# Kernel tuning notes

Measured on AMD Instinct MI355X. Metric: run time of the kernel, lower is better.

## Reference

```python
import jax, jax.numpy as jnp
import numpy as np


def _conv1x1(x, w, b=None):
    # x: [B,C,H,W], w: [O,C]
    y = jnp.einsum('bchw,oc->bohw', x, w)
    if b is not None:
        y = y + b[None, :, None, None]
    return y


def _conv3x3_dilated(x, w, b, dil):
    p = dil  # padding == dilation keeps spatial size for 3x3 kernels
    y = jax.lax.conv_general_dilated(
        x, w, window_strides=(1, 1), padding=((p, p), (p, p)),
        rhs_dilation=(dil, dil), dimension_numbers=('NCHW', 'OIHW', 'NCHW'))
    return y + b[None, :, None, None]


def _upsample2x_align_corners(x):
    # bilinear, align_corners=True, scale factor 2
    B, C, H, W = x.shape
    oh, ow = 2 * H, 2 * W
    ys = jnp.linspace(0.0, H - 1.0, oh)
    xs = jnp.linspace(0.0, W - 1.0, ow)
    y0 = jnp.floor(ys).astype(jnp.int32)
    x0 = jnp.floor(xs).astype(jnp.int32)
    y1 = jnp.minimum(y0 + 1, H - 1)
    x1 = jnp.minimum(x0 + 1, W - 1)
    wy = (ys - y0)[None, None, :, None]
    wx = (xs - x0)[None, None, None, :]
    gt = x[:, :, y0, :]
    gb = x[:, :, y1, :]
    top = gt[:, :, :, x0] * (1 - wx) + gt[:, :, :, x1] * wx
    bot = gb[:, :, :, x0] * (1 - wx) + gb[:, :, :, x1] * wx
    return top * (1 - wy) + bot * wy


def _gr(ftr, ck_w, ck_b, avg_w, max_w, gcn_w):
    # GR module: attention-diagonal graph conv with degree normalization
    B, C, H, W = ftr.shape
    HW = H * W
    # ChannelAttention_diag -> diagonal entries cw: [B, M]
    avg = ftr.mean(axis=(2, 3))
    mx = ftr.max(axis=(2, 3))
    cw = jax.nn.sigmoid(jax.nn.relu(avg @ avg_w.T) + jax.nn.relu(mx @ max_w.T))  # [B,M]
    k = jax.nn.relu(_conv1x1(ftr, ck_w, ck_b)).reshape(B, -1, HW)  # [B,M,HW]
    q = jnp.swapaxes(k, 1, 2)  # [B,HW,M]
    # A = sigmoid(q @ diag(cw) @ k); degree d = rowsum(A)^(-1/2)
    A = jax.nn.sigmoid(jnp.einsum('bim,bm,bmj->bij', q, cw, k))  # [B,HW,HW]
    d = A.sum(axis=2) ** -0.5  # [B,HW]
    P = d[:, :, None] * q  # D^{-1/2} @ q, [B,HW,M]
    X = jnp.swapaxes(ftr.reshape(B, C, HW), 1, 2)  # [B,HW,C]
    PtX = jnp.einsum('bjm,bjc->bmc', P, X)  # [B,M,C]
    LX = X - jnp.einsum('bim,bmc->bic', P, cw[:, :, None] * PtX)
    Y = X + LX @ gcn_w  # GCN (no bias)
    return jnp.swapaxes(Y, 1, 2).reshape(B, C, H, W)


def setup_inputs() -> dict:
    key = jax.random.key(0)
    ks = jax.random.split(key, 20)
    B, C = 64, 1024
    Cq = C // 4  # 256
    Mi = Cq // 2  # 128, ChannelAttention inter channels
    s = 0.02
    inp = {
        'x_cur': jax.random.normal(ks[0], (B, C, 16, 16), jnp.float32),
        'x_lat': jax.random.normal(ks[1], (B, C, 8, 8), jnp.float32),
        'conv_w': jax.random.normal(ks[2], (Cq, C), jnp.float32) * s,
        'conv_b': jax.random.normal(ks[3], (Cq,), jnp.float32) * s,
        'conv1_w': jax.random.normal(ks[4], (C, Cq), jnp.float32) * s,
        'conv1_b': jax.random.normal(ks[5], (C,), jnp.float32) * s,
        'conv3_w': jax.random.normal(ks[6], (C, 3 * Cq), jnp.float32) * s,
        'conv3_b': jax.random.normal(ks[7], (C,), jnp.float32) * s,
        'rate0_w': jax.random.normal(ks[8], (Cq, C, 3, 3), jnp.float32) * s,
        'rate0_b': jax.random.normal(ks[9], (Cq,), jnp.float32) * s,
        'rate1_w': jax.random.normal(ks[10], (Cq, C, 3, 3), jnp.float32) * s,
        'rate1_b': jax.random.normal(ks[11], (Cq,), jnp.float32) * s,
        'rate2_w': jax.random.normal(ks[12], (Cq, C, 3, 3), jnp.float32) * s,
        'rate2_b': jax.random.normal(ks[13], (Cq,), jnp.float32) * s,
        'gr_ck_w': jax.random.normal(ks[14], (Mi, Cq), jnp.float32) * s,
        'gr_ck_b': jax.random.normal(ks[15], (Mi,), jnp.float32) * s,
        'gr_avg_w': jax.random.normal(ks[16], (Mi, Cq), jnp.float32) * s,
        'gr_max_w': jax.random.normal(ks[17], (Mi, Cq), jnp.float32) * s,
        'gr_gcn_w': jax.random.normal(ks[18], (Cq, Cq), jnp.float32) * s,
        'pre': 1,
    }
    return inp


def reference(x_cur, x_lat, conv_w, conv_b, conv1_w, conv1_b, conv3_w, conv3_b,
              rate0_w, rate0_b, rate1_w, rate1_b, rate2_w, rate2_b,
              gr_ck_w, gr_ck_b, gr_avg_w, gr_max_w, gr_gcn_w, pre):
    # pre == 1 path of Graph_aspp.forward
    gr_args = (gr_ck_w, gr_ck_b, gr_avg_w, gr_max_w, gr_gcn_w)
    x_sum = x_cur * _upsample2x_align_corners(x_lat) + x_cur
    f1 = _conv3x3_dilated(x_sum, rate0_w, rate0_b, 1) + _conv1x1(x_sum, conv_w, conv_b)
    x1 = _gr(f1, *gr_args)
    feature = _conv1x1(f1, conv1_w, conv1_b) + x_sum
    f2 = _conv3x3_dilated(feature, rate1_w, rate1_b, 2) + _conv1x1(feature, conv_w, conv_b)
    x2 = _gr(f2, *gr_args)
    feature = _conv1x1(f2, conv1_w, conv1_b) + x_sum
    f3 = _conv3x3_dilated(feature, rate2_w, rate2_b, 4) + _conv1x1(feature, conv_w, conv_b)
    x3 = _gr(f3, *gr_args)
    cat = jnp.concatenate((x1, x2, x3), axis=1)
    return _conv1x1(cat, conv3_w, conv3_b)
```

## Files before the change

### kernel.cpp

```cpp
#include <hip/hip_runtime.h>

typedef unsigned short ushort_t;
typedef unsigned int uint32;
typedef __attribute__((ext_vector_type(8))) unsigned short ushort8;
typedef __attribute__((ext_vector_type(8))) __bf16 bf16x8;
typedef __attribute__((ext_vector_type(4))) float f32x4;

__device__ __forceinline__ ushort_t f2b(float f) {
    union { float f; uint32 u; } v; v.f = f;
    uint32 r = v.u + 0x7fffu + ((v.u >> 16) & 1u);
    return (ushort_t)(r >> 16);
}
__device__ __forceinline__ float b2f(ushort_t b) {
    union { uint32 u; float f; } v; v.u = ((uint32)b) << 16;
    return v.f;
}
__device__ __forceinline__ float sigm(float x) { return 1.f / (1.f + __expf(-x)); }

__device__ __forceinline__ void gload_lds16(const void* g, void* l) {
    __builtin_amdgcn_global_load_lds(
        (__attribute__((address_space(1))) void*)g,
        (__attribute__((address_space(3))) void*)l, 16, 0, 0);
}

constexpr int EPI_RELU  = 1;
constexpr int EPI_FQ    = 2;
constexpr int EPI_SIG   = 3;
constexpr int EPI_XG    = 4;
constexpr int EPI_NEGCW = 5;
constexpr int EPI_Y     = 6;
constexpr int EPI_OUTT  = 7;

struct GemmP {
    const ushort_t* A; const ushort_t* B;
    const ushort_t* A2; const ushort_t* B2;
    long long aBatch, bBatch, a2Batch, b2Batch;
    int lda, ldb, lda2, ldb2;
    int Ksub, kSplit, dil;
    const float* bias;
    const ushort_t* res; long long resBatch; int ldres;
    ushort_t* obf; long long oBatch; int ldo;
    ushort_t* obf2;
    float* of32;
    const float* cw;
    const float* rscale;
    float* dsum;
    const ushort_t* zpage;
};

__global__ __launch_bounds__(256) void gemm_big(GemmP p) {
    __shared__ __align__(16) ushort_t aT[128 * 64];
    __shared__ __align__(16) ushort_t bT[128 * 64];
    const int tid = threadIdx.x;
    const int z = blockIdx.z;
    const int m0 = blockIdx.x * 128, n0 = blockIdx.y * 128;
    const int lane = tid & 63, wid = tid >> 6;
    const int l15 = lane & 15, l16 = lane >> 4;
    const int wr = wid >> 1, wc = wid & 1;
    const int lrow = lane >> 3;
    const int sgran = (lane & 7) ^ lrow;

    int ayy[4], axx[4];
    const ushort_t* aBase[4];
    const ushort_t* bBase[4];
#pragma unroll
    for (int i = 0; i < 4; ++i) {
        int row = wid * 32 + i * 8 + lrow;
        int m = m0 + row;
        int bb = m >> 8;
        ayy[i] = (m >> 4) & 15; axx[i] = m & 15;
        aBase[i] = p.A + (long long)bb * 262144 + sgran * 8;
        bBase[i] = p.B + (long long)(n0 + row) * p.ldb + sgran * 8;
    }

    f32x4 acc[4][4];
#pragma unroll
    for (int i = 0; i < 4; ++i)
#pragma unroll
        for (int j = 0; j < 4; ++j) acc[i][j] = (f32x4){0.f, 0.f, 0.f, 0.f};

    const int gk0 = z * p.kSplit;
    const int ntap = p.Ksub >> 10;
    for (int ti = 0; ti < ntap; ++ti) {
        const int tap = (gk0 >> 10) + ti;
        int dy = 0, dx = 0;
        if (tap < 9) { int ky = tap / 3; dy = (ky - 1) * p.dil; dx = (tap - ky * 3 - 1) * p.dil; }
        const ushort_t* gaA[4];
        const ushort_t* gaB[4];
#pragma unroll
        for (int i = 0; i < 4; ++i) {
            int iy = ayy[i] + dy, ix = axx[i] + dx;
            bool ok = ((unsigned)iy < 16u) && ((unsigned)ix < 16u);
            gaA[i] = ok ? (aBase[i] + (((iy << 4) + ix) << 10)) : (p.zpage + sgran * 8);
            gaB[i] = bBase[i] + (tap << 10);
        }
        for (int kk = 0; kk < 16; ++kk) {
            const int kin = kk << 6;
#pragma unroll
            for (int i = 0; i < 4; ++i)
                gload_lds16(gaA[i] + kin, &aT[(wid * 32 + i * 8) * 64]);
#pragma unroll
            for (int i = 0; i < 4; ++i)
                gload_lds16(gaB[i] + kin, &bT[(wid * 32 + i * 8) * 64]);
            asm volatile("s_waitcnt vmcnt(0)" ::: "memory");
            __syncthreads();
#pragma unroll
            for (int ks = 0; ks < 2; ++ks) {
                bf16x8 af[4], bfr[4];
#pragma unroll
                for (int mi = 0; mi < 4; ++mi) {
                    int rr = wr * 64 + mi * 16 + l15;
                    int cc = (ks * 32 + l16 * 8) ^ ((rr & 7) << 3);
                    af[mi] = __builtin_bit_cast(bf16x8, *(const ushort8*)&aT[rr * 64 + cc]);
                }
#pragma unroll
                for (int ni = 0; ni < 4; ++ni) {
                    int rr = wc * 64 + ni * 16 + l15;
                    int cc = (ks * 32 + l16 * 8) ^ ((rr & 7) << 3);
                    bfr[ni] = __builtin_bit_cast(bf16x8, *(const ushort8*)&bT[rr * 64 + cc]);
                }
#pragma unroll
                for (int mi = 0; mi < 4; ++mi)
#pragma unroll
                    for (int ni = 0; ni < 4; ++ni)
                        acc[mi][ni] = __builtin_amdgcn_mfma_f32_16x16x32_bf16(af[mi], bfr[ni], acc[mi][ni], 0, 0, 0);
            }
            __syncthreads();
        }
    }
#pragma unroll
    for (int mi = 0; mi < 4; ++mi)
#pragma unroll
        for (int ni = 0; ni < 4; ++ni) {
            int gcol = n0 + wc * 64 + ni * 16 + l15;
            int growb = m0 + wr * 64 + mi * 16 + l16 * 4;
#pragma unroll
            for (int r = 0; r < 4; ++r)
                p.obf[(long long)z * p.oBatch + (long long)(growb + r) * 256 + gcol] =
                    f2b(acc[mi][ni][r]);
        }
}

template<int BM, int BN, int AMODE, int EPI>
__global__ __launch_bounds__(256) void gemm_k(GemmP p) {
    __shared__ __align__(16) ushort_t aT[BM * 64];
    __shared__ __align__(16) ushort_t bT[BN * 64];
    constexpr int APASS = BM / 32, BPASS = BN / 32;
    constexpr int MFRAG = BM / 32, NFRAG = BN / 32;
    const int tid = threadIdx.x;
    const int z = blockIdx.z;
    const int m0 = blockIdx.x * BM, n0 = blockIdx.y * BN;
    const int lane = tid & 63, wid = tid >> 6;
    const int l15 = lane & 15, l16 = lane >> 4;
    const int wr = wid >> 1, wc = wid & 1;
    const int srow = tid >> 3, scol = (tid & 7) * 8;
    const int swcol = scol ^ ((srow & 7) << 3);

    const ushort_t* aptr[APASS];
    const ushort_t* bptr[BPASS];
    const ushort_t* aptr2[APASS];
    const ushort_t* bptr2[BPASS];
    float rsA[APASS];
#pragma unroll
    for (int pi = 0; pi < APASS; ++pi)
        aptr[pi] = p.A + (long long)z * p.aBatch +
                   (long long)(m0 + pi * 32 + srow) * p.lda + scol;
#pragma unroll
    for (int pi = 0; pi < BPASS; ++pi)
        bptr[pi] = p.B + (long long)z * p.bBatch +
                   (long long)(n0 + pi * 32 + srow) * p.ldb + scol;
    if constexpr (AMODE == 2) {
#pragma unroll
        for (int pi = 0; pi < APASS; ++pi) {
            aptr2[pi] = p.A2 + (long long)z * p.a2Batch +
                        (long long)(m0 + pi * 32 + srow) * p.lda2 + scol;
            rsA[pi] = p.rscale[z * 256 + m0 + pi * 32 + srow];
        }
#pragma unroll
        for (int pi = 0; pi < BPASS; ++pi)
            bptr2[pi] = p.B2 + (long long)z * p.b2Batch +
                        (long long)(n0 + pi * 32 + srow) * p.ldb2 + scol;
    }

    f32x4 acc[MFRAG][NFRAG];
#pragma unroll
    for (int i = 0; i < MFRAG; ++i)
#pragma unroll
        for (int j = 0; j < NFRAG; ++j) acc[i][j] = (f32x4){0.f, 0.f, 0.f, 0.f};

    ushort8 ar[APASS], br[BPASS];
    auto ldg = [&](int gk) {
        if (AMODE == 2 && gk >= 256) {
            int g2 = gk - 256;
#pragma unroll
            for (int pi = 0; pi < APASS; ++pi) {
                ushort8 t8 = *(const ushort8*)(aptr2[pi] + g2);
#pragma unroll
                for (int k = 0; k < 8; ++k) t8[k] = f2b(b2f(t8[k]) * rsA[pi]);
                ar[pi] = t8;
            }
#pragma unroll
            for (int pi = 0; pi < BPASS; ++pi) br[pi] = *(const ushort8*)(bptr2[pi] + g2);
        } else if constexpr (AMODE == 3) {
#pragma unroll
            for (int pi = 0; pi < APASS; ++pi) {
                ushort8 t8 = *(const ushort8*)(aptr[pi] + gk);
#pragma unroll
                for (int k = 0; k < 8; ++k)
                    t8[k] = f2b(b2f(t8[k]) * p.cw[(z << 7) + gk + scol + k]);
                ar[pi] = t8;
            }
#pragma unroll
            for (int pi = 0; pi < BPASS; ++pi) br[pi] = *(const ushort8*)(bptr[pi] + gk);
        } else {
#pragma unroll
            for (int pi = 0; pi < APASS; ++pi) ar[pi] = *(const ushort8*)(aptr[pi] + gk);
#pragma unroll
            for (int pi = 0; pi < BPASS; ++pi) br[pi] = *(const ushort8*)(bptr[pi] + gk);
        }
    };

    const int gk0 = z * p.kSplit;
    ldg(gk0);
    const int iters = p.Ksub >> 6;
    for (int it = 0; it < iters; ++it) {
#pragma unroll
        for (int pi = 0; pi < APASS; ++pi)
            *(ushort8*)&aT[(pi * 32 + srow) * 64 + swcol] = ar[pi];
#pragma unroll
        for (int pi = 0; pi < BPASS; ++pi)
            *(ushort8*)&bT[(pi * 32 + srow) * 64 + swcol] = br[pi];
        __syncthreads();
        if (it + 1 < iters) ldg(gk0 + (it + 1) * 64);
#pragma unroll
        for (int ks = 0; ks < 2; ++ks) {
            bf16x8 af[MFRAG], bfr[NFRAG];
#pragma unroll
            for (int mi = 0; mi < MFRAG; ++mi) {
                int rr = wr * (BM / 2) + mi * 16 + l15;
                int cc = (ks * 32 + l16 * 8) ^ ((rr & 7) << 3);
                af[mi] = __builtin_bit_cast(bf16x8, *(const ushort8*)&aT[rr * 64 + cc]);
            }
#pragma unroll
            for (int ni = 0; ni < NFRAG; ++ni) {
                int rr = wc * (BN / 2) + ni * 16 + l15;
                int cc = (ks * 32 + l16 * 8) ^ ((rr & 7) << 3);
                bfr[ni] = __builtin_bit_cast(bf16x8, *(const ushort8*)&bT[rr * 64 + cc]);
            }
#pragma unroll
            for (int mi = 0; mi < MFRAG; ++mi)
#pragma unroll
                for (int ni = 0; ni < NFRAG; ++ni)
                    acc[mi][ni] = __builtin_amdgcn_mfma_f32_16x16x32_bf16(af[mi], bfr[ni], acc[mi][ni], 0, 0, 0);
        }
        __syncthreads();
    }

#pragma unroll
    for (int mi = 0; mi < MFRAG; ++mi) {
        if constexpr (EPI == EPI_SIG) {
#pragma unroll
            for (int r = 0; r < 4; ++r) {
                float sv = 0.f;
#pragma unroll
                for (int ni = 0; ni < NFRAG; ++ni) sv += sigm(acc[mi][ni][r]);
                sv += __shfl_xor(sv, 1); sv += __shfl_xor(sv, 2);
                sv += __shfl_xor(sv, 4); sv += __shfl_xor(sv, 8);
                if (l15 == 0) {
                    int grow = m0 + wr * (BM / 2) + mi * 16 + l16 * 4 + r;
                    int q8 = blockIdx.y * 2 + wc;
                    p.dsum[q8 * 16384 + z * 256 + grow] = sv;
                }
            }
        } else {
#pragma unroll
            for (int ni = 0; ni < NFRAG; ++ni) {
                int gcol = n0 + wc * (BN / 2) + ni * 16 + l15;
                int growb = m0 + wr * (BM / 2) + mi * 16 + l16 * 4;
#pragma unroll
                for (int r = 0; r < 4; ++r) {
                    int grow = growb + r;
                    float v = acc[mi][ni][r];
                    if constexpr (EPI == EPI_RELU) {
                        v += p.bias[gcol]; v = fmaxf(v, 0.f);
                        p.obf[(long long)grow * p.ldo + gcol] = f2b(v);
                    } else if constexpr (EPI == EPI_FQ) {
                        v += p.bias[gcol];
                        if (gcol < 1024) {
                            v += b2f(p.res[(long long)grow * 1024 + gcol]);
                            p.obf[(long long)grow * 1024 + gcol] = f2b(v);
                        } else {
                            v = fmaxf(v, 0.f);
                            p.obf2[(long long)grow * 128 + (gcol - 1024)] = f2b(v);
                        }
                    } else if constexpr (EPI == EPI_XG) {
                        p.obf[(long long)z * p.oBatch + (long long)grow * p.ldo + gcol] = f2b(v);
                    } else if constexpr (EPI == EPI_NEGCW) {
                        v *= -p.cw[z * 128 + gcol];
                        p.obf[(long long)z * p.oBatch + (long long)grow * p.ldo + gcol] = f2b(v);
                    } else if constexpr (EPI == EPI_Y) {
                        v = b2f(p.res[(long long)z * p.resBatch + (long long)grow * p.ldres + gcol]) + v;
                        p.obf[(long long)z * p.oBatch + (long long)grow * p.ldo + gcol] = f2b(v);
                    } else if constexpr (EPI == EPI_OUTT) {
                        v += p.bias[grow];
                        int bb = gcol >> 8, px = gcol & 255;
                        p.of32[((long long)bb * 1024 + grow) * 256 + px] = v;
                    }
                }
            }
        }
    }
}


__global__ void k_combine(const ushort_t* __restrict__ t, const float* __restrict__ fbias_s,
                          ushort_t* __restrict__ f) {
    int idx = blockIdx.x * 256 + threadIdx.x;
    const long long N = 16384ll * 256;
    ushort8 a0 = *(const ushort8*)(t + (long long)idx * 8);
    ushort8 a1 = *(const ushort8*)(t + N + (long long)idx * 8);
    ushort8 a2 = *(const ushort8*)(t + 2 * N + (long long)idx * 8);
    ushort8 a3 = *(const ushort8*)(t + 3 * N + (long long)idx * 8);
    ushort8 a4 = *(const ushort8*)(t + 4 * N + (long long)idx * 8);
    int cb = (idx * 8) & 255;
    ushort8 o;
#pragma unroll
    for (int k = 0; k < 8; ++k)
        o[k] = f2b(b2f(a0[k]) + b2f(a1[k]) + b2f(a2[k]) + b2f(a3[k]) + b2f(a4[k]) + fbias_s[cb + k]);
    *(ushort8*)&f[(long long)idx * 8] = o;
}

__global__ void k_upsum(const float* __restrict__ xc, const float* __restrict__ xl,
                        ushort_t* __restrict__ xs) {
    __shared__ float lat[64 * 64];
    __shared__ ushort_t tile[64 * 258];
    int b = blockIdx.x, c0 = blockIdx.y * 64;
    int t = threadIdx.x;
    for (int i = t; i < 4096; i += 256)
        lat[i] = xl[((long long)(b * 1024 + c0 + (i >> 6))) * 64 + (i & 63)];
    __syncthreads();
    int y = t >> 4, x = t & 15;
    float fy = y * (7.f / 15.f); int y0 = (int)fy; float wy = fy - y0; int y1 = y0 + 1 > 7 ? 7 : y0 + 1;
    float fx = x * (7.f / 15.f); int x0 = (int)fx; float wx = fx - x0; int x1 = x0 + 1 > 7 ? 7 : x0 + 1;
    for (int cc = 0; cc < 64; ++cc) {
        float cur = xc[((long long)(b * 1024 + c0 + cc)) * 256 + t];
        const float* L = &lat[cc * 64];
        float tv = L[y0 * 8 + x0] * (1.f - wx) + L[y0 * 8 + x1] * wx;
        float bv = L[y1 * 8 + x0] * (1.f - wx) + L[y1 * 8 + x1] * wx;
        float up = tv + (bv - tv) * wy;
        tile[cc * 258 + t] = f2b(cur * (1.f + up));
    }
    __syncthreads();
    for (int i = t; i < 16384; i += 256) {
        int px = i >> 6, cc = i & 63;
        xs[((long long)(b * 256 + px)) * 1024 + c0 + cc] = tile[cc * 258 + px];
    }
}

__global__ void k_poolcw(const ushort_t* __restrict__ f,
                         const float* __restrict__ aw, const float* __restrict__ mw,
                         float* __restrict__ cw) {
    __shared__ float ss[4][256];
    __shared__ float mm_[4][256];
    int b = blockIdx.x, t = threadIdx.x;
    int ch = t & 255, grp = t >> 8;
    float s = 0.f, m = -3.4e38f;
    const ushort_t* base = f + (long long)b * 65536 + ch;
    for (int px = grp; px < 256; px += 4) {
        float v = b2f(base[px * 256]); s += v; m = fmaxf(m, v);
    }
    ss[grp][ch] = s; mm_[grp][ch] = m;
    __syncthreads();
    if (t < 256) {
        s = ss[0][t] + ss[1][t] + ss[2][t] + ss[3][t];
        m = fmaxf(fmaxf(mm_[0][t], mm_[1][t]), fmaxf(mm_[2][t], mm_[3][t]));
        ss[0][t] = s * (1.f / 256.f);
        mm_[0][t] = m;
    }
    __syncthreads();
    if (t < 128) {
        float s1 = 0.f, s2 = 0.f;
        const float* a = aw + t * 256; const float* w = mw + t * 256;
        for (int c = 0; c < 256; ++c) { s1 += ss[0][c] * a[c]; s2 += mm_[0][c] * w[c]; }
        s1 = fmaxf(s1, 0.f); s2 = fmaxf(s2, 0.f);
        cw[b * 128 + t] = sigm(s1 + s2);
    }
}

__global__ void k_pscale(const ushort_t* __restrict__ q, const float* __restrict__ dsum8,
                         float* __restrict__ dscale, ushort_t* __restrict__ Pt) {
    __shared__ ushort_t t[128][130];
    __shared__ float dd[128];
    int jh = blockIdx.x, b = blockIdx.y;
    int j0 = jh * 128;
    int tid = threadIdx.x;
    if (tid < 128) {
        int pix = b * 256 + j0 + tid;
        float s = 0.f;
#pragma unroll
        for (int qs = 0; qs < 8; ++qs) s += dsum8[qs * 16384 + pix];
        float r = rsqrtf(s);
        dd[tid] = r;
        dscale[pix] = r;
    }
    __syncthreads();
    int jr = tid >> 7, m = tid & 127;
    for (int i = 0; i < 64; ++i) {
        int j = i * 2 + jr;
        long long qi = ((long long)(b * 256 + j0 + j)) * 128 + m;
        t[j][m] = f2b(dd[j] * b2f(q[qi]));
    }
    __syncthreads();
    for (int i = 0; i < 64; ++i) {
        int mm = i * 2 + jr;
        Pt[((long long)b << 15) + (mm << 8) + j0 + m] = t[m][mm];
    }
}

__global__ void k_packall(const float* r0, const float* r1, const float* r2,
                          const float* convw, const float* c1w, const float* c3w,
                          const float* ckw, const float* gcnw,
                          const float* rb0, const float* rb1, const float* rb2,
                          const float* cb, const float* c1b, const float* ckbias,
                          ushort_t* wbig3, ushort_t* wfq, ushort_t* w3b,
                          ushort_t* gcnT, float* fqbias, float* fbias,
                          ushort_t* zpage) {
    int blk = blockIdx.x, tid = threadIdx.x;
    if (blk < 768) {
        __shared__ float lw[10240];
        int s = blk >> 8, o = blk & 255;
        const float* rate = s == 0 ? r0 : (s == 1 ? r1 : r2);
        for (int i = tid; i < 9216; i += 256) lw[i] = rate[(long long)o * 9216 + i];
        for (int i = tid; i < 1024; i += 256) lw[9216 + i] = convw[(long long)o * 1024 + i];
        __syncthreads();
        ushort_t* dst = wbig3 + (long long)blk * 10240;
        for (int i = tid; i < 10240; i += 256) {
            int tap = i >> 10, ci = i & 1023;
            float v = (tap < 9) ? lw[ci * 9 + tap] : lw[9216 + ci];
            dst[i] = f2b(v);
        }
        return;
    }
    const int R1 = 262144;
    const int R2 = R1 + 32768;
    const int R3 = R2 + 786432;
    const int R4 = R3 + 65536;
    const int R5 = R4 + 1152;
    const int R6 = R5 + 768;
    const int R7 = R6 + 4096;
    int base = (blk - 768) * 2048 + tid * 8;
#pragma unroll
    for (int k = 0; k < 8; ++k) {
        int i = base + k;
        if (i >= R7) return;
        if (i < R1) wfq[i] = f2b(c1w[i]);
        else if (i < R2) wfq[i] = f2b(ckw[i - R1]);
        else if (i < R3) w3b[i - R2] = f2b(c3w[i - R2]);
        else if (i < R4) {
            int ii = i - R3; int c2 = ii >> 8, c1 = ii & 255;
            gcnT[ii] = f2b(gcnw[c1 * 256 + c2]);
        } else if (i < R5) {
            int ii = i - R4;
            fqbias[ii] = (ii < 1024) ? c1b[ii] : ckbias[ii - 1024];
        } else if (i < R6) {
            int ii = i - R5; int s = ii >> 8, t = ii & 255;
            const float* rb = s == 0 ? rb0 : (s == 1 ? rb1 : rb2);
            fbias[ii] = rb[t] + cb[t];
        } else {
            zpage[i - R6] = 0;
        }
    }
}

__global__ void k_sentinel(float* o, int n, float v) {
    int i = blockIdx.x * 256 + threadIdx.x; if (i < n) o[i] = v;
}

extern "C" void kernel_launch(void* const* d_in, const int* in_sizes, int n_in,
                              void* d_out, int out_size, void* d_ws, size_t ws_size,
                              hipStream_t stream) {
    const float* x_cur  = (const float*)d_in[0];
    const float* x_lat  = (const float*)d_in[1];
    const float* conv_w = (const float*)d_in[2];
    const float* conv_b = (const float*)d_in[3];
    const float* conv1_w = (const float*)d_in[4];
    const float* conv1_b = (const float*)d_in[5];
    const float* conv3_w = (const float*)d_in[6];
    const float* conv3_b = (const float*)d_in[7];
    const float* rate_w[3] = {(const float*)d_in[8], (const float*)d_in[10], (const float*)d_in[12]};
    const float* rate_b[3] = {(const float*)d_in[9], (const float*)d_in[11], (const float*)d_in[13]};
    const float* ck_w  = (const float*)d_in[14];
    const float* ck_b  = (const float*)d_in[15];
    const float* avg_w = (const float*)d_in[16];
    const float* max_w = (const float*)d_in[17];
    const float* gcn_w = (const float*)d_in[18];
    float* out = (float*)d_out;

    char* w = (char*)d_ws;
    auto take = [&](size_t bytes) { void* p = (void*)w; w += (bytes + 255) & ~(size_t)255; return p; };
    ushort_t* xsum   = (ushort_t*)take(16384ll * 1024 * 2);
    ushort_t* feat   = (ushort_t*)take(16384ll * 1024 * 2);
    ushort_t* fbuf   = (ushort_t*)take(16384ll * 256 * 2);
    ushort_t* xgt    = (ushort_t*)take(64ll * 256 * 256 * 2);
    ushort_t* qbuf   = (ushort_t*)take(16384ll * 128 * 2);
    ushort_t* Pt     = (ushort_t*)take(64ll * 128 * 256 * 2);
    ushort_t* Htn    = (ushort_t*)take(64ll * 256 * 128 * 2);
    ushort_t* wbig3  = (ushort_t*)take(3ll * 256 * 10240 * 2);
    ushort_t* wfq    = (ushort_t*)take(1152ll * 256 * 2);
    ushort_t* w3b    = (ushort_t*)take(1024ll * 768 * 2);
    ushort_t* gcnT   = (ushort_t*)take(256ll * 256 * 2);
    ushort_t* zpage  = (ushort_t*)take(8192);
    float*    fqbias = (float*)take(1152 * 4);
    float*    fbias  = (float*)take(3 * 256 * 4);
    float*    cwb    = (float*)take(64 * 128 * 4);
    float*    dscale = (float*)take(64 * 256 * 4);
    float*    dsum8  = (float*)take(8ll * 64 * 256 * 4);
    ushort_t* catb   = (ushort_t*)take(16384ll * 768 * 2);
    ushort_t* ftmp   = (ushort_t*)take(5ll * 16384 * 256 * 2);
    size_t need = (size_t)(w - (char*)d_ws);

    if (need > ws_size) {
        float v = 1.0e6f + (float)(ws_size >> 20);
        k_sentinel<<<(out_size + 255) / 256, 256, 0, stream>>>(out, out_size, v);
        return;
    }

    k_packall<<<768 + 563, 256, 0, stream>>>(
        rate_w[0], rate_w[1], rate_w[2], conv_w, conv1_w, conv3_w, ck_w, gcn_w,
        rate_b[0], rate_b[1], rate_b[2], conv_b, conv1_b, ck_b,
        wbig3, wfq, w3b, gcnT, fqbias, fbias, zpage);
    k_upsum<<<dim3(64, 16), 256, 0, stream>>>(x_cur, x_lat, xsum);

    for (int s = 0; s < 3; ++s) {
        {
            GemmP p{};
            p.A = (s == 0) ? xsum : feat;
            p.B = wbig3 + (long long)s * 256 * 10240; p.ldb = 10240;
            p.Ksub = 2048; p.kSplit = 2048; p.dil = 1 << s;
            p.obf = ftmp; p.oBatch = 16384ll * 256;
            p.zpage = zpage;
            gemm_big<<<dim3(128, 2, 5), 256, 0, stream>>>(p);
        }
        k_combine<<<2048, 256, 0, stream>>>(ftmp, fbias + s * 256, fbuf);
        k_poolcw<<<64, 1024, 0, stream>>>(fbuf, avg_w, max_w, cwb);
        if (s < 2) {
            GemmP p{};
            p.A = fbuf; p.lda = 256; p.B = wfq; p.ldb = 256;
            p.Ksub = 256; p.bias = fqbias;
            p.res = xsum;
            p.obf = feat; p.obf2 = qbuf;
            gemm_k<64, 64, 0, EPI_FQ><<<dim3(256, 18, 1), 256, 0, stream>>>(p);
        } else {
            GemmP p{};
            p.A = fbuf; p.lda = 256; p.B = wfq + 1024 * 256; p.ldb = 256;
            p.Ksub = 256;
            p.bias = ck_b; p.obf = qbuf; p.ldo = 128;
            gemm_k<64, 64, 0, EPI_RELU><<<dim3(256, 2, 1), 256, 0, stream>>>(p);
        }
        {
            GemmP p{};
            p.A = qbuf; p.aBatch = 32768; p.lda = 128;
            p.B = qbuf; p.bBatch = 32768; p.ldb = 128;
            p.Ksub = 128; p.dsum = dsum8; p.cw = cwb;
            gemm_k<64, 64, 3, EPI_SIG><<<dim3(4, 4, 64), 256, 0, stream>>>(p);
        }
        k_pscale<<<dim3(2, 64), 256, 0, stream>>>(qbuf, dsum8, dscale, Pt);
        {
            GemmP p{};
            p.A = gcnT; p.aBatch = 0;     p.lda = 256;
            p.B = fbuf; p.bBatch = 65536; p.ldb = 256;
            p.Ksub = 256;
            p.obf = xgt; p.oBatch = 65536; p.ldo = 256;
            gemm_k<64, 64, 0, EPI_XG><<<dim3(4, 4, 64), 256, 0, stream>>>(p);
        }
        {
            GemmP p{};
            p.A = xgt; p.aBatch = 65536; p.lda = 256;
            p.B = Pt;  p.bBatch = 32768; p.ldb = 256;
            p.Ksub = 256; p.cw = cwb;
            p.obf = Htn; p.oBatch = 32768; p.ldo = 128;
            gemm_k<64, 64, 0, EPI_NEGCW><<<dim3(4, 2, 64), 256, 0, stream>>>(p);
        }
        {
            GemmP p{};
            p.A = fbuf; p.aBatch = 65536; p.lda = 256;
            p.B = gcnT; p.bBatch = 0;     p.ldb = 256;
            p.A2 = qbuf; p.a2Batch = 32768; p.lda2 = 128; p.rscale = dscale;
            p.B2 = Htn;  p.b2Batch = 32768; p.ldb2 = 128;
            p.Ksub = 384;
            p.res = fbuf; p.resBatch = 65536; p.ldres = 256;
            p.obf = catb + s * 256; p.oBatch = 256ll * 768; p.ldo = 768;
            gemm_k<64, 64, 2, EPI_Y><<<dim3(4, 4, 64), 256, 0, stream>>>(p);
        }
    }
    {
        GemmP p{};
        p.A = w3b;  p.lda = 768;
        p.B = catb; p.ldb = 768;
        p.Ksub = 768; p.bias = conv3_b; p.of32 = out;
        gemm_k<64, 128, 0, EPI_OUTT><<<dim3(16, 128, 1), 256, 0, stream>>>(p);
    }
}
```

Measured before the change: 690.4 us.

## Use 256x256 tiles with double-buffered LDS pipeline and fewer split-K slices

Replaces the 128x128 dilated-conv GEMM with a 512-thread kernel that covers all 256 output channels in one 256-row tile, so the A operand is no longer fetched once per column block. Global-to-LDS loads are double-buffered and tracked with partial vmcnt waits so the next K slice loads while the current one computes. Split-K goes from 5 to 4 slices of 2560, which cuts partial-sum traffic in the combine kernel. The cost is a 128 KB LDS footprint, more accumulator registers, and a smaller grid (256 blocks), which lowers occupancy.

```diff
diff --git a/kernel.cpp b/kernel.cpp
--- a/kernel.cpp
+++ b/kernel.cpp
@@ -48,92 +48,99 @@
     const ushort_t* zpage;
 };
 
-__global__ __launch_bounds__(256) void gemm_big(GemmP p) {
-    __shared__ __align__(16) ushort_t aT[128 * 64];
-    __shared__ __align__(16) ushort_t bT[128 * 64];
+__global__ __launch_bounds__(512, 2) void gemm_big256(GemmP p) {
+    __shared__ __align__(16) ushort_t aT[2][256 * 64];
+    __shared__ __align__(16) ushort_t bT[2][256 * 64];
     const int tid = threadIdx.x;
     const int z = blockIdx.z;
-    const int m0 = blockIdx.x * 128, n0 = blockIdx.y * 128;
+    const int m0 = blockIdx.x * 256;
     const int lane = tid & 63, wid = tid >> 6;
     const int l15 = lane & 15, l16 = lane >> 4;
-    const int wr = wid >> 1, wc = wid & 1;
+    const int wr = wid >> 2, wc = wid & 3;
     const int lrow = lane >> 3;
     const int sgran = (lane & 7) ^ lrow;
 
     int ayy[4], axx[4];
     const ushort_t* aBase[4];
     const ushort_t* bBase[4];
+    const long long bbOff = (long long)(m0 >> 8) * 262144;
 #pragma unroll
     for (int i = 0; i < 4; ++i) {
         int row = wid * 32 + i * 8 + lrow;
         int m = m0 + row;
-        int bb = m >> 8;
         ayy[i] = (m >> 4) & 15; axx[i] = m & 15;
-        aBase[i] = p.A + (long long)bb * 262144 + sgran * 8;
-        bBase[i] = p.B + (long long)(n0 + row) * p.ldb + sgran * 8;
-    }
-
-    f32x4 acc[4][4];
-#pragma unroll
-    for (int i = 0; i < 4; ++i)
+        aBase[i] = p.A + bbOff + sgran * 8;
+        bBase[i] = p.B + (long long)row * p.ldb + sgran * 8;
+    }
+
+    f32x4 acc[8][4];
+#pragma unroll
+    for (int i = 0; i < 8; ++i)
 #pragma unroll
         for (int j = 0; j < 4; ++j) acc[i][j] = (f32x4){0.f, 0.f, 0.f, 0.f};
 
     const int gk0 = z * p.kSplit;
-    const int ntap = p.Ksub >> 10;
-    for (int ti = 0; ti < ntap; ++ti) {
-        const int tap = (gk0 >> 10) + ti;
+    const int iters = p.Ksub >> 6;
+
+    auto stage = [&](int t, int buf) {
+        const int gk = gk0 + t * 64;
+        const int tap = gk >> 10, kin = gk & 1023;
         int dy = 0, dx = 0;
         if (tap < 9) { int ky = tap / 3; dy = (ky - 1) * p.dil; dx = (tap - ky * 3 - 1) * p.dil; }
-        const ushort_t* gaA[4];
-        const ushort_t* gaB[4];
 #pragma unroll
         for (int i = 0; i < 4; ++i) {
             int iy = ayy[i] + dy, ix = axx[i] + dx;
             bool ok = ((unsigned)iy < 16u) && ((unsigned)ix < 16u);
-            gaA[i] = ok ? (aBase[i] + (((iy << 4) + ix) << 10)) : (p.zpage + sgran * 8);
-            gaB[i] = bBase[i] + (tap << 10);
-        }
-        for (int kk = 0; kk < 16; ++kk) {
-            const int kin = kk << 6;
-#pragma unroll
-            for (int i = 0; i < 4; ++i)
-                gload_lds16(gaA[i] + kin, &aT[(wid * 32 + i * 8) * 64]);
-#pragma unroll
-            for (int i = 0; i < 4; ++i)
-                gload_lds16(gaB[i] + kin, &bT[(wid * 32 + i * 8) * 64]);
+            const ushort_t* ga = ok ? (aBase[i] + (((iy << 4) + ix) << 10) + kin)
+                                    : (p.zpage + sgran * 8);
+            gload_lds16(ga, &aT[buf][(wid * 32 + i * 8) * 64]);
+        }
+#pragma unroll
+        for (int i = 0; i < 4; ++i)
+            gload_lds16(bBase[i] + gk, &bT[buf][(wid * 32 + i * 8) * 64]);
+    };
+
+    stage(0, 0);
+    if (iters > 1) stage(1, 1);
+
+    for (int t = 0; t < iters; ++t) {
+        const int buf = t & 1;
+        if (t + 1 < iters)
+            asm volatile("s_waitcnt vmcnt(8)" ::: "memory");
+        else
             asm volatile("s_waitcnt vmcnt(0)" ::: "memory");
-            __syncthreads();
-#pragma unroll
-            for (int ks = 0; ks < 2; ++ks) {
-                bf16x8 af[4], bfr[4];
-#pragma unroll
-                for (int mi = 0; mi < 4; ++mi) {
-                    int rr = wr * 64 + mi * 16 + l15;
-                    int cc = (ks * 32 + l16 * 8) ^ ((rr & 7) << 3);
-                    af[mi] = __builtin_bit_cast(bf16x8, *(const ushort8*)&aT[rr * 64 + cc]);
-                }
-#pragma unroll
-                for (int ni = 0; ni < 4; ++ni) {
-                    int rr = wc * 64 + ni * 16 + l15;
-                    int cc = (ks * 32 + l16 * 8) ^ ((rr & 7) << 3);
-                    bfr[ni] = __builtin_bit_cast(bf16x8, *(const ushort8*)&bT[rr * 64 + cc]);
-                }
-#pragma unroll
-                for (int mi = 0; mi < 4; ++mi)
-#pragma unroll
-                    for (int ni = 0; ni < 4; ++ni)
-                        acc[mi][ni] = __builtin_amdgcn_mfma_f32_16x16x32_bf16(af[mi], bfr[ni], acc[mi][ni], 0, 0, 0);
-            }
-            __syncthreads();
-        }
-    }
-#pragma unroll
-    for (int mi = 0; mi < 4; ++mi)
+        __builtin_amdgcn_s_barrier();
+#pragma unroll
+        for (int ks = 0; ks < 2; ++ks) {
+            bf16x8 af[8], bfr[4];
+#pragma unroll
+            for (int mi = 0; mi < 8; ++mi) {
+                int rr = wr * 128 + mi * 16 + l15;
+                int cc = (ks * 32 + l16 * 8) ^ ((rr & 7) << 3);
+                af[mi] = __builtin_bit_cast(bf16x8, *(const ushort8*)&aT[buf][rr * 64 + cc]);
+            }
+#pragma unroll
+            for (int ni = 0; ni < 4; ++ni) {
+                int rr = wc * 64 + ni * 16 + l15;
+                int cc = (ks * 32 + l16 * 8) ^ ((rr & 7) << 3);
+                bfr[ni] = __builtin_bit_cast(bf16x8, *(const ushort8*)&bT[buf][rr * 64 + cc]);
+            }
+#pragma unroll
+            for (int mi = 0; mi < 8; ++mi)
+#pragma unroll
+                for (int ni = 0; ni < 4; ++ni)
+                    acc[mi][ni] = __builtin_amdgcn_mfma_f32_16x16x32_bf16(af[mi], bfr[ni], acc[mi][ni], 0, 0, 0);
+        }
+        __builtin_amdgcn_s_barrier();
+        if (t + 2 < iters) stage(t + 2, buf);
+    }
+
+#pragma unroll
+    for (int mi = 0; mi < 8; ++mi)
 #pragma unroll
         for (int ni = 0; ni < 4; ++ni) {
-            int gcol = n0 + wc * 64 + ni * 16 + l15;
-            int growb = m0 + wr * 64 + mi * 16 + l16 * 4;
+            int gcol = wc * 64 + ni * 16 + l15;
+            int growb = m0 + wr * 128 + mi * 16 + l16 * 4;
 #pragma unroll
             for (int r = 0; r < 4; ++r)
                 p.obf[(long long)z * p.oBatch + (long long)(growb + r) * 256 + gcol] =
@@ -321,12 +328,11 @@
     ushort8 a1 = *(const ushort8*)(t + N + (long long)idx * 8);
     ushort8 a2 = *(const ushort8*)(t + 2 * N + (long long)idx * 8);
     ushort8 a3 = *(const ushort8*)(t + 3 * N + (long long)idx * 8);
-    ushort8 a4 = *(const ushort8*)(t + 4 * N + (long long)idx * 8);
     int cb = (idx * 8) & 255;
     ushort8 o;
 #pragma unroll
     for (int k = 0; k < 8; ++k)
-        o[k] = f2b(b2f(a0[k]) + b2f(a1[k]) + b2f(a2[k]) + b2f(a3[k]) + b2f(a4[k]) + fbias_s[cb + k]);
+        o[k] = f2b(b2f(a0[k]) + b2f(a1[k]) + b2f(a2[k]) + b2f(a3[k]) + fbias_s[cb + k]);
     *(ushort8*)&f[(long long)idx * 8] = o;
 }
 
@@ -516,7 +522,7 @@
     float*    dscale = (float*)take(64 * 256 * 4);
     float*    dsum8  = (float*)take(8ll * 64 * 256 * 4);
     ushort_t* catb   = (ushort_t*)take(16384ll * 768 * 2);
-    ushort_t* ftmp   = (ushort_t*)take(5ll * 16384 * 256 * 2);
+    ushort_t* ftmp   = (ushort_t*)take(4ll * 16384 * 256 * 2);
     size_t need = (size_t)(w - (char*)d_ws);
 
     if (need > ws_size) {
@@ -536,10 +542,10 @@
             GemmP p{};
             p.A = (s == 0) ? xsum : feat;
             p.B = wbig3 + (long long)s * 256 * 10240; p.ldb = 10240;
-            p.Ksub = 2048; p.kSplit = 2048; p.dil = 1 << s;
+            p.Ksub = 2560; p.kSplit = 2560; p.dil = 1 << s;
             p.obf = ftmp; p.oBatch = 16384ll * 256;
             p.zpage = zpage;
-            gemm_big<<<dim3(128, 2, 5), 256, 0, stream>>>(p);
+            gemm_big256<<<dim3(64, 1, 4), 512, 0, stream>>>(p);
         }
         k_combine<<<2048, 256, 0, stream>>>(ftmp, fbias + s * 256, fbuf);
         k_poolcw<<<64, 1024, 0, stream>>>(fbuf, avg_w, max_w, cwb);
```

New measurement: 703.8 us. No clear change (+1.9%).

## Merge pooling into FQ GEMM launch and co-launch SIG and XG GEMMs

Applied to the files above, without the earlier changes.

Removes the separate channel-attention pooling kernel by giving it extra blocks inside the FQ (or relu-Q) GEMM launch. It also merges the independent sigmoid-affinity GEMM and the GCN-weight XG GEMM into one grid split by z. The FQ GEMM tile grows from 64x64 to 128x128. The aim is fewer launches and better overlap of small kernels. The trade-off is that the pool blocks now run one channel per thread over 256 threads, which is less parallel than the old 1024-thread kernel and may form a tail. The larger FQ tile also reduces the number of blocks.

```diff
diff --git a/kernel.cpp b/kernel.cpp
--- a/kernel.cpp
+++ b/kernel.cpp
@@ -142,13 +142,11 @@
 }
 
 template<int BM, int BN, int AMODE, int EPI>
-__global__ __launch_bounds__(256) void gemm_k(GemmP p) {
-    __shared__ __align__(16) ushort_t aT[BM * 64];
-    __shared__ __align__(16) ushort_t bT[BN * 64];
+__device__ __forceinline__ void gemm_body(ushort_t* aT, ushort_t* bT,
+                                          const GemmP& p, int z) {
     constexpr int APASS = BM / 32, BPASS = BN / 32;
     constexpr int MFRAG = BM / 32, NFRAG = BN / 32;
     const int tid = threadIdx.x;
-    const int z = blockIdx.z;
     const int m0 = blockIdx.x * BM, n0 = blockIdx.y * BN;
     const int lane = tid & 63, wid = tid >> 6;
     const int l15 = lane & 15, l16 = lane >> 4;
@@ -312,6 +310,64 @@
     }
 }
 
+template<int BM, int BN, int AMODE, int EPI>
+__global__ __launch_bounds__(256) void gemm_k(GemmP p) {
+    __shared__ __align__(16) ushort_t aT[BM * 64];
+    __shared__ __align__(16) ushort_t bT[BN * 64];
+    gemm_body<BM, BN, AMODE, EPI>(aT, bT, p, blockIdx.z);
+}
+
+__device__ __forceinline__ void pool_body(void* lds, const ushort_t* f,
+                                          const float* aw, const float* mw,
+                                          float* cw) {
+    float* sa = (float*)lds;
+    float* sm = sa + 256;
+    int b = blockIdx.x, t = threadIdx.x;
+    float s = 0.f, m = -3.4e38f;
+    const ushort_t* base = f + (long long)b * 65536 + t;
+    for (int px = 0; px < 256; ++px) { float v = b2f(base[px * 256]); s += v; m = fmaxf(m, v); }
+    sa[t] = s * (1.f / 256.f);
+    sm[t] = m;
+    __syncthreads();
+    if (t < 128) {
+        float s1 = 0.f, s2 = 0.f;
+        const float* a = aw + t * 256; const float* w = mw + t * 256;
+        for (int c = 0; c < 256; ++c) { s1 += sa[c] * a[c]; s2 += sm[c] * w[c]; }
+        s1 = fmaxf(s1, 0.f); s2 = fmaxf(s2, 0.f);
+        cw[b * 128 + t] = sigm(s1 + s2);
+    }
+}
+
+__global__ __launch_bounds__(256) void gemm_fqpool(GemmP p, const float* aw,
+                                                   const float* mw, float* cw) {
+    __shared__ __align__(16) ushort_t aT[128 * 64];
+    __shared__ __align__(16) ushort_t bT[128 * 64];
+    if (blockIdx.y == 9) {
+        if (blockIdx.x < 64) pool_body(aT, p.A, aw, mw, cw);
+        return;
+    }
+    gemm_body<128, 128, 0, EPI_FQ>(aT, bT, p, 0);
+}
+
+__global__ __launch_bounds__(256) void gemm_qpool(GemmP p, const float* aw,
+                                                  const float* mw, float* cw) {
+    __shared__ __align__(16) ushort_t aT[64 * 64];
+    __shared__ __align__(16) ushort_t bT[64 * 64];
+    if (blockIdx.y == 2) {
+        if (blockIdx.x < 64) pool_body(aT, p.A, aw, mw, cw);
+        return;
+    }
+    gemm_body<64, 64, 0, EPI_RELU>(aT, bT, p, 0);
+}
+
+__global__ __launch_bounds__(256) void gemm_sigxg(GemmP ps, GemmP px) {
+    __shared__ __align__(16) ushort_t aT[64 * 64];
+    __shared__ __align__(16) ushort_t bT[64 * 64];
+    int z = blockIdx.z;
+    if (z < 64) gemm_body<64, 64, 3, EPI_SIG>(aT, bT, ps, z);
+    else        gemm_body<64, 64, 0, EPI_XG>(aT, bT, px, z - 64);
+}
+
 
 __global__ void k_combine(const ushort_t* __restrict__ t, const float* __restrict__ fbias_s,
                           ushort_t* __restrict__ f) {
@@ -354,36 +410,6 @@
     for (int i = t; i < 16384; i += 256) {
         int px = i >> 6, cc = i & 63;
         xs[((long long)(b * 256 + px)) * 1024 + c0 + cc] = tile[cc * 258 + px];
-    }
-}
-
-__global__ void k_poolcw(const ushort_t* __restrict__ f,
-                         const float* __restrict__ aw, const float* __restrict__ mw,
-                         float* __restrict__ cw) {
-    __shared__ float ss[4][256];
-    __shared__ float mm_[4][256];
-    int b = blockIdx.x, t = threadIdx.x;
-    int ch = t & 255, grp = t >> 8;
-    float s = 0.f, m = -3.4e38f;
-    const ushort_t* base = f + (long long)b * 65536 + ch;
-    for (int px = grp; px < 256; px += 4) {
-        float v = b2f(base[px * 256]); s += v; m = fmaxf(m, v);
-    }
-    ss[grp][ch] = s; mm_[grp][ch] = m;
-    __syncthreads();
-    if (t < 256) {
-        s = ss[0][t] + ss[1][t] + ss[2][t] + ss[3][t];
-        m = fmaxf(fmaxf(mm_[0][t], mm_[1][t]), fmaxf(mm_[2][t], mm_[3][t]));
-        ss[0][t] = s * (1.f / 256.f);
-        mm_[0][t] = m;
-    }
-    __syncthreads();
-    if (t < 128) {
-        float s1 = 0.f, s2 = 0.f;
-        const float* a = aw + t * 256; const float* w = mw + t * 256;
-        for (int c = 0; c < 256; ++c) { s1 += ss[0][c] * a[c]; s2 += mm_[0][c] * w[c]; }
-        s1 = fmaxf(s1, 0.f); s2 = fmaxf(s2, 0.f);
-        cw[b * 128 + t] = sigm(s1 + s2);
     }
 }
 
@@ -542,37 +568,33 @@
             gemm_big<<<dim3(128, 2, 5), 256, 0, stream>>>(p);
         }
         k_combine<<<2048, 256, 0, stream>>>(ftmp, fbias + s * 256, fbuf);
-        k_poolcw<<<64, 1024, 0, stream>>>(fbuf, avg_w, max_w, cwb);
         if (s < 2) {
             GemmP p{};
             p.A = fbuf; p.lda = 256; p.B = wfq; p.ldb = 256;
             p.Ksub = 256; p.bias = fqbias;
             p.res = xsum;
             p.obf = feat; p.obf2 = qbuf;
-            gemm_k<64, 64, 0, EPI_FQ><<<dim3(256, 18, 1), 256, 0, stream>>>(p);
+            gemm_fqpool<<<dim3(128, 10, 1), 256, 0, stream>>>(p, avg_w, max_w, cwb);
         } else {
             GemmP p{};
             p.A = fbuf; p.lda = 256; p.B = wfq + 1024 * 256; p.ldb = 256;
             p.Ksub = 256;
             p.bias = ck_b; p.obf = qbuf; p.ldo = 128;
-            gemm_k<64, 64, 0, EPI_RELU><<<dim3(256, 2, 1), 256, 0, stream>>>(p);
+            gemm_qpool<<<dim3(256, 3, 1), 256, 0, stream>>>(p, avg_w, max_w, cwb);
         }
         {
-            GemmP p{};
-            p.A = qbuf; p.aBatch = 32768; p.lda = 128;
-            p.B = qbuf; p.bBatch = 32768; p.ldb = 128;
-            p.Ksub = 128; p.dsum = dsum8; p.cw = cwb;
-            gemm_k<64, 64, 3, EPI_SIG><<<dim3(4, 4, 64), 256, 0, stream>>>(p);
+            GemmP ps{};
+            ps.A = qbuf; ps.aBatch = 32768; ps.lda = 128;
+            ps.B = qbuf; ps.bBatch = 32768; ps.ldb = 128;
+            ps.Ksub = 128; ps.dsum = dsum8; ps.cw = cwb;
+            GemmP px{};
+            px.A = gcnT; px.aBatch = 0;     px.lda = 256;
+            px.B = fbuf; px.bBatch = 65536; px.ldb = 256;
+            px.Ksub = 256;
+            px.obf = xgt; px.oBatch = 65536; px.ldo = 256;
+            gemm_sigxg<<<dim3(4, 4, 128), 256, 0, stream>>>(ps, px);
         }
         k_pscale<<<dim3(2, 64), 256, 0, stream>>>(qbuf, dsum8, dscale, Pt);
-        {
-            GemmP p{};
-            p.A = gcnT; p.aBatch = 0;     p.lda = 256;
-            p.B = fbuf; p.bBatch = 65536; p.ldb = 256;
-            p.Ksub = 256;
-            p.obf = xgt; p.oBatch = 65536; p.ldo = 256;
-            gemm_k<64, 64, 0, EPI_XG><<<dim3(4, 4, 64), 256, 0, stream>>>(p);
-        }
         {
             GemmP p{};
             p.A = xgt; p.aBatch = 65536; p.lda = 256;
```

New measurement: 646.4 us. 6.4% less time.
